# Optimization experiments

Measured on AMD Instinct MI355X. Metric: run time of the kernel, lower is better.

Reference implementation:

```python
import jax, jax.numpy as jnp
import numpy as np

E = 8        # num experts
K = 2        # top-k
H = 1024     # hidden size
F = 3584     # intermediate (ffn) size
B, S = 1, 2048


def setup_inputs() -> dict:
    key = jax.random.key(0)
    ks = jax.random.split(key, 5)
    scale_h = 1.0 / np.sqrt(H)
    scale_f = 1.0 / np.sqrt(F)
    return {
        "hidden_states": jax.random.normal(ks[0], (B, S, H), jnp.float32),
        "gate_w": jax.random.normal(ks[1], (E, H), jnp.float32) * scale_h,  # Linear [out,in]
        "w1": jax.random.normal(ks[2], (E, F, H), jnp.float32) * scale_h,
        "w3": jax.random.normal(ks[3], (E, F, H), jnp.float32) * scale_h,
        "w2": jax.random.normal(ks[4], (E, H, F), jnp.float32) * scale_f,
    }


def reference(hidden_states, gate_w, w1, w3, w2):
    b, s, h = hidden_states.shape
    x = hidden_states.reshape(-1, h)                       # [T,H]
    T = x.shape[0]
    # Router: softmax over experts, top-k, renormalize
    router_logits = x @ gate_w.T                           # [T,E]
    routing_weights = jax.nn.softmax(router_logits.astype(jnp.float32), axis=-1)
    topk_w, topk_idx = jax.lax.top_k(routing_weights, K)   # [T,K]
    topk_w = topk_w / jnp.sum(topk_w, axis=-1, keepdims=True)
    # Per-token, per-expert combine weight (0 for unselected experts) --
    # matches the original mask-and-sum over all experts.
    tok = jnp.arange(T)
    expert_weights = jnp.zeros((T, E), jnp.float32).at[tok[:, None], topk_idx].add(topk_w)  # [T,E]
    # Dense per-expert SiLU-gated MLP over all tokens (as the reference loop does),
    # vectorized across experts.
    g = jnp.einsum("th,efh->etf", x, w1)                   # [E,T,F]
    u = jnp.einsum("th,efh->etf", x, w3)                   # [E,T,F]
    act = jax.nn.silu(g) * u                               # [E,T,F]
    y = jnp.einsum("etf,ehf->eth", act, w2)                # [E,T,H]
    out = jnp.einsum("eth,te->th", y, expert_weights.astype(y.dtype))  # [T,H]
    return out.reshape(b, s, h)
```

## Files before the change

kernel.cpp:

```cpp
#include <hip/hip_runtime.h>
#include <hip/hip_bf16.h>

#define T_TOK 2048
#define HID   1024
#define FF    3584
#define NE    8
#define TOPK  2
#define GRIDY 24

typedef __bf16 bf16x8 __attribute__((ext_vector_type(8)));
typedef float  f32x4  __attribute__((ext_vector_type(4)));
typedef unsigned short u16x8 __attribute__((ext_vector_type(8)));

#define WS_COUNTS   0u
#define WS_OFFSETS  64u
#define WS_TILECNT  128u
#define WS_TLE      256u
#define WS_TLM      512u
#define WS_TOPKI    4096u
#define WS_TOPKW    20480u
#define WS_SLOTPOS  36864u
#define WS_SLOTROW  53248u
#define WS_ROUTETOK 69632u
#define WS_XG       131072u
#define WS_ACT      (WS_XG + 4096u*1024u*2u)
#define WS_Y        (WS_ACT + 4096u*3584u*2u)
#define Y_STRIDE    (4096u*1024u)

static __device__ __forceinline__ unsigned short f2bf(float f) {
    unsigned int u = __builtin_bit_cast(unsigned int, f);
    u += 0x7FFFu + ((u >> 16) & 1u);
    return (unsigned short)(u >> 16);
}
static __device__ __forceinline__ unsigned int cvtpk(float lo, float hi) {
    unsigned int r;
    asm("v_cvt_pk_bf16_f32 %0, %1, %2" : "=v"(r) : "v"(lo), "v"(hi));
    return r;
}

__global__ __launch_bounds__(256) void k_router(
    const float* __restrict__ x, const float* __restrict__ gw,
    int* __restrict__ counts, int* __restrict__ topki,
    float* __restrict__ topkw, int* __restrict__ slotpos)
{
    int t = blockIdx.x * 4 + (threadIdx.x >> 6);
    int l = threadIdx.x & 63;
    const float* xr = x + (size_t)t * HID;
    float acc[NE];
#pragma unroll
    for (int e = 0; e < NE; ++e) acc[e] = 0.f;
#pragma unroll
    for (int i = 0; i < 4; ++i) {
        int h = l * 4 + i * 256;
        float4 xv = *(const float4*)(xr + h);
#pragma unroll
        for (int e = 0; e < NE; ++e) {
            float4 g = *(const float4*)(gw + e * HID + h);
            acc[e] += xv.x * g.x + xv.y * g.y + xv.z * g.z + xv.w * g.w;
        }
    }
#pragma unroll
    for (int e = 0; e < NE; ++e) {
#pragma unroll
        for (int off = 32; off; off >>= 1) acc[e] += __shfl_xor(acc[e], off);
    }
    if (l == 0) {
        float best = -1e30f, second = -1e30f;
        int bi = 0, si = 0;
#pragma unroll
        for (int e = 0; e < NE; ++e) {
            float v = acc[e];
            if (v > best) { second = best; si = bi; best = v; bi = e; }
            else if (v > second) { second = v; si = e; }
        }
        float w0 = 1.f / (1.f + __expf(second - best));
        float w1 = 1.f - w0;
        topki[2 * t] = bi;  topki[2 * t + 1] = si;
        topkw[2 * t] = w0;  topkw[2 * t + 1] = w1;
        slotpos[2 * t]     = atomicAdd(&counts[bi], 1);
        slotpos[2 * t + 1] = atomicAdd(&counts[si], 1);
    }
}

__global__ void k_prefix(const int* __restrict__ counts, int* __restrict__ offsets,
                         int* __restrict__ tle, int* __restrict__ tlm,
                         int* __restrict__ tilecnt) {
    if (threadIdx.x == 0) {
        int o = 0;
#pragma unroll
        for (int e = 0; e < NE; ++e) { offsets[e] = o; o += counts[e]; }
        int n = 0;
        for (int e = 0; e < NE; ++e) {
            int t = (counts[e] + 255) >> 8;
            for (int i = 0; i < t; ++i) { tle[n] = e; tlm[n] = i; ++n; }
        }
        tilecnt[0] = n;
    }
}

__global__ void k_fill(const int* __restrict__ topki, const int* __restrict__ slotpos,
                       const int* __restrict__ offsets, int* __restrict__ routetok,
                       int* __restrict__ slotrow) {
    int j = blockIdx.x * blockDim.x + threadIdx.x;
    if (j >= T_TOK * TOPK) return;
    int e = topki[j];
    int row = offsets[e] + slotpos[j];
    routetok[row] = j >> 1;
    slotrow[j] = row;
}

__global__ void k_gather(const float* __restrict__ x, const int* __restrict__ routetok,
                         unsigned short* __restrict__ xg) {
    int j = blockIdx.x * blockDim.x + threadIdx.x;
    int r = j >> 8;
    int c = (j & 255) * 4;
    int tok = routetok[r];
    float4 v = *(const float4*)(x + (size_t)tok * HID + c);
    ushort4 o;
    o.x = f2bf(v.x); o.y = f2bf(v.y); o.z = f2bf(v.z); o.w = f2bf(v.w);
    int sc = c ^ ((r & 7) << 3);
    *(ushort4*)(xg + (size_t)r * HID + sc) = o;
}

__global__ __launch_bounds__(512, 4) void k_gemm1(
    const unsigned short* __restrict__ xg, const float* __restrict__ w1,
    const float* __restrict__ w3, const int* __restrict__ counts,
    const int* __restrict__ offsets, const int* __restrict__ tle,
    const int* __restrict__ tlm, const int* __restrict__ tilecnt,
    unsigned short* __restrict__ act)
{
    int by = blockIdx.y;
    if (by >= tilecnt[0]) return;
    int e = tle[by];
    int rbase = tlm[by] * 256;
    int cnt = counts[e], obase = offsets[e];
    int fbase = blockIdx.x * 64;

    __shared__ __align__(16) unsigned short lA[256 * 64];
    __shared__ __align__(16) unsigned short lB1[64 * 64];
    __shared__ __align__(16) unsigned short lB3[64 * 64];

    int tid = threadIdx.x;
    const int ra0 = tid >> 3, ca = (tid & 7) * 8;
    const int rb0 = tid >> 4, cb = (tid & 15) * 4;
    const unsigned short* pa[4];
#pragma unroll
    for (int i = 0; i < 4; ++i) {
        int r = obase + rbase + ra0 + 64 * i;
        if (r > 4095) r = 4095;
        pa[i] = xg + (size_t)r * HID + ca;
    }
    const float* w1e = w1 + ((size_t)e * FF + fbase) * HID;
    const float* w3e = w3 + ((size_t)e * FF + fbase) * HID;
    const float* pb1[2];
    const float* pb3[2];
    int wba[2];
#pragma unroll
    for (int i = 0; i < 2; ++i) {
        int row = rb0 + 32 * i;
        pb1[i] = w1e + (size_t)row * HID + cb;
        pb3[i] = w3e + (size_t)row * HID + cb;
        wba[i] = row * 64 + (cb ^ ((row & 7) << 3));
    }

    int lane = tid & 63, wv = tid >> 6, wr = wv >> 1, wc = wv & 1;
    int klane = (lane >> 4) * 8;
    int swzA = (((obase & 7) + (lane & 7)) & 7) << 3;
    int swzB = (lane & 7) << 3;
    f32x4 accg[4][2], accu[4][2];
#pragma unroll
    for (int m = 0; m < 4; ++m)
#pragma unroll
        for (int n = 0; n < 2; ++n) {
            accg[m][n] = (f32x4){0.f, 0.f, 0.f, 0.f};
            accu[m][n] = (f32x4){0.f, 0.f, 0.f, 0.f};
        }

    u16x8 ra[4]; float4 r1[2], r3[2];
#pragma unroll
    for (int i = 0; i < 4; ++i) ra[i] = *(const u16x8*)(pa[i]);
#pragma unroll
    for (int i = 0; i < 2; ++i) { r1[i] = *(const float4*)(pb1[i]); r3[i] = *(const float4*)(pb3[i]); }

    for (int kt = 0; kt < HID / 64; ++kt) {
#pragma unroll
        for (int i = 0; i < 4; ++i)
            *(u16x8*)(lA + (ra0 + 64 * i) * 64 + ca) = ra[i];
#pragma unroll
        for (int i = 0; i < 2; ++i) {
            uint2 p;
            p.x = cvtpk(r1[i].x, r1[i].y); p.y = cvtpk(r1[i].z, r1[i].w);
            *(uint2*)(lB1 + wba[i]) = p;
            p.x = cvtpk(r3[i].x, r3[i].y); p.y = cvtpk(r3[i].z, r3[i].w);
            *(uint2*)(lB3 + wba[i]) = p;
        }
        __syncthreads();
        if (kt < HID / 64 - 1) {
            int kof = (kt + 1) * 64;
#pragma unroll
            for (int i = 0; i < 4; ++i) ra[i] = *(const u16x8*)(pa[i] + kof);
#pragma unroll
            for (int i = 0; i < 2; ++i) {
                r1[i] = *(const float4*)(pb1[i] + kof);
                r3[i] = *(const float4*)(pb3[i] + kof);
            }
        }
#pragma unroll
        for (int kk = 0; kk < 64; kk += 32) {
            int kc = kk + klane;
            int kA = kc ^ swzA, kB = kc ^ swzB;
            bf16x8 a[4], b1[2], b3[2];
#pragma unroll
            for (int m = 0; m < 4; ++m)
                a[m] = *(const bf16x8*)(lA + (wr * 64 + m * 16 + (lane & 15)) * 64 + kA);
#pragma unroll
            for (int n = 0; n < 2; ++n) {
                b1[n] = *(const bf16x8*)(lB1 + (wc * 32 + n * 16 + (lane & 15)) * 64 + kB);
                b3[n] = *(const bf16x8*)(lB3 + (wc * 32 + n * 16 + (lane & 15)) * 64 + kB);
            }
#pragma unroll
            for (int m = 0; m < 4; ++m)
#pragma unroll
                for (int n = 0; n < 2; ++n) {
                    accg[m][n] = __builtin_amdgcn_mfma_f32_16x16x32_bf16(a[m], b1[n], accg[m][n], 0, 0, 0);
                    accu[m][n] = __builtin_amdgcn_mfma_f32_16x16x32_bf16(a[m], b3[n], accu[m][n], 0, 0, 0);
                }
        }
        __syncthreads();
    }

#pragma unroll
    for (int m = 0; m < 4; ++m)
#pragma unroll
        for (int n = 0; n < 2; ++n)
#pragma unroll
            for (int r = 0; r < 4; ++r) {
                int lr = wr * 64 + m * 16 + (lane >> 4) * 4 + r;
                if (rbase + lr < cnt) {
                    float g = accg[m][n][r], u = accu[m][n][r];
                    float s = g / (1.f + __expf(-g));
                    int row = obase + rbase + lr;
                    int col = fbase + wc * 32 + n * 16 + (lane & 15);
                    int scol = col ^ ((row & 7) << 3);
                    act[(size_t)row * FF + scol] = f2bf(s * u);
                }
            }
}

__global__ __launch_bounds__(512, 4) void k_gemm2(
    const unsigned short* __restrict__ act, const float* __restrict__ w2,
    const int* __restrict__ counts, const int* __restrict__ offsets,
    const int* __restrict__ tle, const int* __restrict__ tlm,
    const int* __restrict__ tilecnt, float* __restrict__ y)
{
    int by = blockIdx.y;
    if (by >= tilecnt[0]) return;
    int e = tle[by];
    int rbase = tlm[by] * 256;
    int cnt = counts[e], obase = offsets[e];
    int hbase = blockIdx.x * 64;
    int z = blockIdx.z;
    const int kb0 = z * (FF / 2);
    const int KS = FF / 2 / 64;

    __shared__ __align__(16) unsigned short lA[256 * 64];
    __shared__ __align__(16) unsigned short lB[64 * 64];

    int tid = threadIdx.x;
    const int ra0 = tid >> 3, ca = (tid & 7) * 8;
    const int rb0 = tid >> 4, cb = (tid & 15) * 4;
    const unsigned short* pa[4];
#pragma unroll
    for (int i = 0; i < 4; ++i) {
        int r = obase + rbase + ra0 + 64 * i;
        if (r > 4095) r = 4095;
        pa[i] = act + (size_t)r * FF + kb0 + ca;
    }
    const float* w2e = w2 + ((size_t)e * HID + hbase) * FF;
    const float* pb[2];
    int wba[2];
#pragma unroll
    for (int i = 0; i < 2; ++i) {
        int row = rb0 + 32 * i;
        pb[i] = w2e + (size_t)row * FF + kb0 + cb;
        wba[i] = row * 64 + (cb ^ ((row & 7) << 3));
    }

    int lane = tid & 63, wv = tid >> 6, wr = wv >> 1, wc = wv & 1;
    int klane = (lane >> 4) * 8;
    int swzA = (((obase & 7) + (lane & 7)) & 7) << 3;
    int swzB = (lane & 7) << 3;
    f32x4 acc[4][2];
#pragma unroll
    for (int m = 0; m < 4; ++m)
#pragma unroll
        for (int n = 0; n < 2; ++n) acc[m][n] = (f32x4){0.f, 0.f, 0.f, 0.f};

    u16x8 ra[4]; float4 rw[2];
#pragma unroll
    for (int i = 0; i < 4; ++i) ra[i] = *(const u16x8*)(pa[i]);
#pragma unroll
    for (int i = 0; i < 2; ++i) rw[i] = *(const float4*)(pb[i]);

    for (int kt = 0; kt < KS; ++kt) {
#pragma unroll
        for (int i = 0; i < 4; ++i)
            *(u16x8*)(lA + (ra0 + 64 * i) * 64 + ca) = ra[i];
#pragma unroll
        for (int i = 0; i < 2; ++i) {
            uint2 p;
            p.x = cvtpk(rw[i].x, rw[i].y); p.y = cvtpk(rw[i].z, rw[i].w);
            *(uint2*)(lB + wba[i]) = p;
        }
        __syncthreads();
        if (kt < KS - 1) {
            int kof = (kt + 1) * 64;
#pragma unroll
            for (int i = 0; i < 4; ++i) ra[i] = *(const u16x8*)(pa[i] + kof);
#pragma unroll
            for (int i = 0; i < 2; ++i) rw[i] = *(const float4*)(pb[i] + kof);
        }
#pragma unroll
        for (int kk = 0; kk < 64; kk += 32) {
            int kc = kk + klane;
            int kA = kc ^ swzA, kB = kc ^ swzB;
            bf16x8 a[4], b[2];
#pragma unroll
            for (int m = 0; m < 4; ++m)
                a[m] = *(const bf16x8*)(lA + (wr * 64 + m * 16 + (lane & 15)) * 64 + kA);
#pragma unroll
            for (int n = 0; n < 2; ++n)
                b[n] = *(const bf16x8*)(lB + (wc * 32 + n * 16 + (lane & 15)) * 64 + kB);
#pragma unroll
            for (int m = 0; m < 4; ++m)
#pragma unroll
                for (int n = 0; n < 2; ++n)
                    acc[m][n] = __builtin_amdgcn_mfma_f32_16x16x32_bf16(a[m], b[n], acc[m][n], 0, 0, 0);
        }
        __syncthreads();
    }

    float* yz = y + (size_t)z * Y_STRIDE;
#pragma unroll
    for (int m = 0; m < 4; ++m)
#pragma unroll
        for (int n = 0; n < 2; ++n)
#pragma unroll
            for (int r = 0; r < 4; ++r) {
                int lr = wr * 64 + m * 16 + (lane >> 4) * 4 + r;
                if (rbase + lr < cnt) {
                    int col = hbase + wc * 32 + n * 16 + (lane & 15);
                    yz[(size_t)(obase + rbase + lr) * HID + col] = acc[m][n][r];
                }
            }
}

__global__ void k_combine(const float* __restrict__ y, const int* __restrict__ slotrow,
                          const float* __restrict__ topkw, float* __restrict__ out) {
    int j = blockIdx.x * blockDim.x + threadIdx.x;
    int t = j >> 8, c = j & 255;
    int r0 = slotrow[2 * t], r1 = slotrow[2 * t + 1];
    float w0 = topkw[2 * t], w1 = topkw[2 * t + 1];
    const float4* y0 = (const float4*)y;
    const float4* y1 = (const float4*)(y + (size_t)Y_STRIDE);
    float4 a0 = y0[(size_t)r0 * 256 + c], a1 = y1[(size_t)r0 * 256 + c];
    float4 b0 = y0[(size_t)r1 * 256 + c], b1 = y1[(size_t)r1 * 256 + c];
    float4 o;
    o.x = w0 * (a0.x + a1.x) + w1 * (b0.x + b1.x);
    o.y = w0 * (a0.y + a1.y) + w1 * (b0.y + b1.y);
    o.z = w0 * (a0.z + a1.z) + w1 * (b0.z + b1.z);
    o.w = w0 * (a0.w + a1.w) + w1 * (b0.w + b1.w);
    ((float4*)out)[j] = o;
}

extern "C" void kernel_launch(void* const* d_in, const int* in_sizes, int n_in,
                              void* d_out, int out_size, void* d_ws, size_t ws_size,
                              hipStream_t stream) {
    const float* x  = (const float*)d_in[0];
    const float* gw = (const float*)d_in[1];
    const float* w1 = (const float*)d_in[2];
    const float* w3 = (const float*)d_in[3];
    const float* w2 = (const float*)d_in[4];
    float* out = (float*)d_out;

    char* ws = (char*)d_ws;
    int*   counts   = (int*)(ws + WS_COUNTS);
    int*   offsets  = (int*)(ws + WS_OFFSETS);
    int*   tilecnt  = (int*)(ws + WS_TILECNT);
    int*   tle      = (int*)(ws + WS_TLE);
    int*   tlm      = (int*)(ws + WS_TLM);
    int*   topki    = (int*)(ws + WS_TOPKI);
    float* topkw    = (float*)(ws + WS_TOPKW);
    int*   slotpos  = (int*)(ws + WS_SLOTPOS);
    int*   slotrow  = (int*)(ws + WS_SLOTROW);
    int*   routetok = (int*)(ws + WS_ROUTETOK);
    unsigned short* xg   = (unsigned short*)(ws + WS_XG);
    unsigned short* actb = (unsigned short*)(ws + WS_ACT);
    float* yb = (float*)(ws + WS_Y);

    hipMemsetAsync(counts, 0, 64, stream);
    k_router<<<T_TOK / 4, 256, 0, stream>>>(x, gw, counts, topki, topkw, slotpos);
    k_prefix<<<1, 64, 0, stream>>>(counts, offsets, tle, tlm, tilecnt);
    k_fill<<<16, 256, 0, stream>>>(topki, slotpos, offsets, routetok, slotrow);
    k_gather<<<4096, 256, 0, stream>>>(x, routetok, xg);
    k_gemm1<<<dim3(FF / 64, GRIDY, 1), 512, 0, stream>>>(xg, w1, w3, counts, offsets, tle, tlm, tilecnt, actb);
    k_gemm2<<<dim3(HID / 64, GRIDY, 2), 512, 0, stream>>>(actb, w2, counts, offsets, tle, tlm, tilecnt, yb);
    k_combine<<<2048, 256, 0, stream>>>(yb, slotrow, topkw, out);
}
```

Before: 279.0 us.

## Retile gemm2 to 128x128 tiles with configurable split-K

The down-projection kernel changes from 256x64 tiles with 512 threads to 128x128 tiles with 256 threads. It uses a separate 128-row tile list built in the prefix kernel and a split-K factor of 4 when the workspace is large enough. Each thread now loads 32 contiguous fp32 weights per k-step and writes them to LDS as packed 16-byte bf16 stores. The aim is to cut redundant w2 loads per output and add more blocks for occupancy. In exchange, the combine kernel must read and sum more partial y buffers.

```diff
diff --git a/kernel.cpp b/kernel.cpp
--- a/kernel.cpp
+++ b/kernel.cpp
@@ -6,7 +6,8 @@
 #define FF    3584
 #define NE    8
 #define TOPK  2
-#define GRIDY 24
+#define GRIDY1 24
+#define GRIDY2 40
 
 typedef __bf16 bf16x8 __attribute__((ext_vector_type(8)));
 typedef float  f32x4  __attribute__((ext_vector_type(4)));
@@ -15,8 +16,10 @@
 #define WS_COUNTS   0u
 #define WS_OFFSETS  64u
 #define WS_TILECNT  128u
-#define WS_TLE      256u
-#define WS_TLM      512u
+#define WS_TLE1     256u
+#define WS_TLM1     512u
+#define WS_TLE2     768u
+#define WS_TLM2     1024u
 #define WS_TOPKI    4096u
 #define WS_TOPKW    20480u
 #define WS_SLOTPOS  36864u
@@ -83,18 +86,21 @@
 }
 
 __global__ void k_prefix(const int* __restrict__ counts, int* __restrict__ offsets,
-                         int* __restrict__ tle, int* __restrict__ tlm,
+                         int* __restrict__ tl1e, int* __restrict__ tl1m,
+                         int* __restrict__ tl2e, int* __restrict__ tl2m,
                          int* __restrict__ tilecnt) {
     if (threadIdx.x == 0) {
         int o = 0;
 #pragma unroll
         for (int e = 0; e < NE; ++e) { offsets[e] = o; o += counts[e]; }
-        int n = 0;
+        int n1 = 0, n2 = 0;
         for (int e = 0; e < NE; ++e) {
-            int t = (counts[e] + 255) >> 8;
-            for (int i = 0; i < t; ++i) { tle[n] = e; tlm[n] = i; ++n; }
-        }
-        tilecnt[0] = n;
+            int t1 = (counts[e] + 255) >> 8;
+            for (int i = 0; i < t1; ++i) { tl1e[n1] = e; tl1m[n1] = i; ++n1; }
+            int t2 = (counts[e] + 127) >> 7;
+            for (int i = 0; i < t2; ++i) { tl2e[n2] = e; tl2m[n2] = i; ++n2; }
+        }
+        tilecnt[0] = n1; tilecnt[1] = n2;
     }
 }
 
@@ -247,94 +253,96 @@
             }
 }
 
-__global__ __launch_bounds__(512, 4) void k_gemm2(
+__global__ __launch_bounds__(256, 4) void k_gemm2(
     const unsigned short* __restrict__ act, const float* __restrict__ w2,
     const int* __restrict__ counts, const int* __restrict__ offsets,
     const int* __restrict__ tle, const int* __restrict__ tlm,
-    const int* __restrict__ tilecnt, float* __restrict__ y)
+    const int* __restrict__ tilecnt, float* __restrict__ y, int ks)
 {
     int by = blockIdx.y;
-    if (by >= tilecnt[0]) return;
+    if (by >= tilecnt[1]) return;
     int e = tle[by];
-    int rbase = tlm[by] * 256;
+    int rbase = tlm[by] * 128;
     int cnt = counts[e], obase = offsets[e];
-    int hbase = blockIdx.x * 64;
+    int hbase = blockIdx.x * 128;
     int z = blockIdx.z;
-    const int kb0 = z * (FF / 2);
-    const int KS = FF / 2 / 64;
-
-    __shared__ __align__(16) unsigned short lA[256 * 64];
-    __shared__ __align__(16) unsigned short lB[64 * 64];
+    const int KTOT = FF / 64;
+    int per = (KTOT + ks - 1) / ks;
+    int kt0 = z * per;
+    int ktn = (KTOT < kt0 + per ? KTOT : kt0 + per) - kt0;
+    int kb0 = kt0 * 64;
+
+    __shared__ __align__(16) unsigned short lA[128 * 64];
+    __shared__ __align__(16) unsigned short lB[128 * 64];
 
     int tid = threadIdx.x;
     const int ra0 = tid >> 3, ca = (tid & 7) * 8;
-    const int rb0 = tid >> 4, cb = (tid & 15) * 4;
     const unsigned short* pa[4];
 #pragma unroll
     for (int i = 0; i < 4; ++i) {
-        int r = obase + rbase + ra0 + 64 * i;
+        int r = obase + rbase + ra0 + 32 * i;
         if (r > 4095) r = 4095;
         pa[i] = act + (size_t)r * FF + kb0 + ca;
     }
-    const float* w2e = w2 + ((size_t)e * HID + hbase) * FF;
-    const float* pb[2];
-    int wba[2];
-#pragma unroll
-    for (int i = 0; i < 2; ++i) {
-        int row = rb0 + 32 * i;
-        pb[i] = w2e + (size_t)row * FF + kb0 + cb;
-        wba[i] = row * 64 + (cb ^ ((row & 7) << 3));
-    }
+    int hr = tid >> 1, kh = tid & 1;
+    const float* pb = w2 + ((size_t)e * HID + hbase + hr) * FF + kb0 + kh * 32;
+    int wba[4];
+#pragma unroll
+    for (int g = 0; g < 4; ++g)
+        wba[g] = hr * 64 + ((kh * 32 + g * 8) ^ ((hr & 7) << 3));
 
     int lane = tid & 63, wv = tid >> 6, wr = wv >> 1, wc = wv & 1;
     int klane = (lane >> 4) * 8;
     int swzA = (((obase & 7) + (lane & 7)) & 7) << 3;
     int swzB = (lane & 7) << 3;
-    f32x4 acc[4][2];
+    f32x4 acc[4][4];
 #pragma unroll
     for (int m = 0; m < 4; ++m)
 #pragma unroll
-        for (int n = 0; n < 2; ++n) acc[m][n] = (f32x4){0.f, 0.f, 0.f, 0.f};
-
-    u16x8 ra[4]; float4 rw[2];
+        for (int n = 0; n < 4; ++n) acc[m][n] = (f32x4){0.f, 0.f, 0.f, 0.f};
+
+    u16x8 ra[4]; float4 rw[8];
 #pragma unroll
     for (int i = 0; i < 4; ++i) ra[i] = *(const u16x8*)(pa[i]);
 #pragma unroll
-    for (int i = 0; i < 2; ++i) rw[i] = *(const float4*)(pb[i]);
-
-    for (int kt = 0; kt < KS; ++kt) {
+    for (int j = 0; j < 8; ++j) rw[j] = *(const float4*)(pb + 4 * j);
+
+    for (int kt = 0; kt < ktn; ++kt) {
 #pragma unroll
         for (int i = 0; i < 4; ++i)
-            *(u16x8*)(lA + (ra0 + 64 * i) * 64 + ca) = ra[i];
-#pragma unroll
-        for (int i = 0; i < 2; ++i) {
-            uint2 p;
-            p.x = cvtpk(rw[i].x, rw[i].y); p.y = cvtpk(rw[i].z, rw[i].w);
-            *(uint2*)(lB + wba[i]) = p;
+            *(u16x8*)(lA + (ra0 + 32 * i) * 64 + ca) = ra[i];
+#pragma unroll
+        for (int g = 0; g < 4; ++g) {
+            uint4 q;
+            q.x = cvtpk(rw[2 * g].x, rw[2 * g].y);
+            q.y = cvtpk(rw[2 * g].z, rw[2 * g].w);
+            q.z = cvtpk(rw[2 * g + 1].x, rw[2 * g + 1].y);
+            q.w = cvtpk(rw[2 * g + 1].z, rw[2 * g + 1].w);
+            *(uint4*)(lB + wba[g]) = q;
         }
         __syncthreads();
-        if (kt < KS - 1) {
+        if (kt < ktn - 1) {
             int kof = (kt + 1) * 64;
 #pragma unroll
             for (int i = 0; i < 4; ++i) ra[i] = *(const u16x8*)(pa[i] + kof);
 #pragma unroll
-            for (int i = 0; i < 2; ++i) rw[i] = *(const float4*)(pb[i] + kof);
+            for (int j = 0; j < 8; ++j) rw[j] = *(const float4*)(pb + kof + 4 * j);
         }
 #pragma unroll
         for (int kk = 0; kk < 64; kk += 32) {
             int kc = kk + klane;
             int kA = kc ^ swzA, kB = kc ^ swzB;
-            bf16x8 a[4], b[2];
+            bf16x8 a[4], b[4];
 #pragma unroll
             for (int m = 0; m < 4; ++m)
                 a[m] = *(const bf16x8*)(lA + (wr * 64 + m * 16 + (lane & 15)) * 64 + kA);
 #pragma unroll
-            for (int n = 0; n < 2; ++n)
-                b[n] = *(const bf16x8*)(lB + (wc * 32 + n * 16 + (lane & 15)) * 64 + kB);
+            for (int n = 0; n < 4; ++n)
+                b[n] = *(const bf16x8*)(lB + (wc * 64 + n * 16 + (lane & 15)) * 64 + kB);
 #pragma unroll
             for (int m = 0; m < 4; ++m)
 #pragma unroll
-                for (int n = 0; n < 2; ++n)
+                for (int n = 0; n < 4; ++n)
                     acc[m][n] = __builtin_amdgcn_mfma_f32_16x16x32_bf16(a[m], b[n], acc[m][n], 0, 0, 0);
         }
         __syncthreads();
@@ -344,32 +352,36 @@
 #pragma unroll
     for (int m = 0; m < 4; ++m)
 #pragma unroll
-        for (int n = 0; n < 2; ++n)
+        for (int n = 0; n < 4; ++n)
 #pragma unroll
             for (int r = 0; r < 4; ++r) {
                 int lr = wr * 64 + m * 16 + (lane >> 4) * 4 + r;
                 if (rbase + lr < cnt) {
-                    int col = hbase + wc * 32 + n * 16 + (lane & 15);
+                    int col = hbase + wc * 64 + n * 16 + (lane & 15);
                     yz[(size_t)(obase + rbase + lr) * HID + col] = acc[m][n][r];
                 }
             }
 }
 
 __global__ void k_combine(const float* __restrict__ y, const int* __restrict__ slotrow,
-                          const float* __restrict__ topkw, float* __restrict__ out) {
+                          const float* __restrict__ topkw, float* __restrict__ out, int ks) {
     int j = blockIdx.x * blockDim.x + threadIdx.x;
     int t = j >> 8, c = j & 255;
     int r0 = slotrow[2 * t], r1 = slotrow[2 * t + 1];
     float w0 = topkw[2 * t], w1 = topkw[2 * t + 1];
-    const float4* y0 = (const float4*)y;
-    const float4* y1 = (const float4*)(y + (size_t)Y_STRIDE);
-    float4 a0 = y0[(size_t)r0 * 256 + c], a1 = y1[(size_t)r0 * 256 + c];
-    float4 b0 = y0[(size_t)r1 * 256 + c], b1 = y1[(size_t)r1 * 256 + c];
+    float4 a = {0.f, 0.f, 0.f, 0.f}, b = {0.f, 0.f, 0.f, 0.f};
+    for (int z = 0; z < ks; ++z) {
+        const float4* yz = (const float4*)(y + (size_t)z * Y_STRIDE);
+        float4 av = yz[(size_t)r0 * 256 + c];
+        float4 bv = yz[(size_t)r1 * 256 + c];
+        a.x += av.x; a.y += av.y; a.z += av.z; a.w += av.w;
+        b.x += bv.x; b.y += bv.y; b.z += bv.z; b.w += bv.w;
+    }
     float4 o;
-    o.x = w0 * (a0.x + a1.x) + w1 * (b0.x + b1.x);
-    o.y = w0 * (a0.y + a1.y) + w1 * (b0.y + b1.y);
-    o.z = w0 * (a0.z + a1.z) + w1 * (b0.z + b1.z);
-    o.w = w0 * (a0.w + a1.w) + w1 * (b0.w + b1.w);
+    o.x = w0 * a.x + w1 * b.x;
+    o.y = w0 * a.y + w1 * b.y;
+    o.z = w0 * a.z + w1 * b.z;
+    o.w = w0 * a.w + w1 * b.w;
     ((float4*)out)[j] = o;
 }
 
@@ -387,8 +399,10 @@
     int*   counts   = (int*)(ws + WS_COUNTS);
     int*   offsets  = (int*)(ws + WS_OFFSETS);
     int*   tilecnt  = (int*)(ws + WS_TILECNT);
-    int*   tle      = (int*)(ws + WS_TLE);
-    int*   tlm      = (int*)(ws + WS_TLM);
+    int*   tl1e     = (int*)(ws + WS_TLE1);
+    int*   tl1m     = (int*)(ws + WS_TLM1);
+    int*   tl2e     = (int*)(ws + WS_TLE2);
+    int*   tl2m     = (int*)(ws + WS_TLM2);
     int*   topki    = (int*)(ws + WS_TOPKI);
     float* topkw    = (float*)(ws + WS_TOPKW);
     int*   slotpos  = (int*)(ws + WS_SLOTPOS);
@@ -398,12 +412,15 @@
     unsigned short* actb = (unsigned short*)(ws + WS_ACT);
     float* yb = (float*)(ws + WS_Y);
 
+    size_t ybytes = (size_t)Y_STRIDE * 4;
+    int ks = (ws_size >= (size_t)WS_Y + 4 * ybytes) ? 4 : 2;
+
     hipMemsetAsync(counts, 0, 64, stream);
     k_router<<<T_TOK / 4, 256, 0, stream>>>(x, gw, counts, topki, topkw, slotpos);
-    k_prefix<<<1, 64, 0, stream>>>(counts, offsets, tle, tlm, tilecnt);
+    k_prefix<<<1, 64, 0, stream>>>(counts, offsets, tl1e, tl1m, tl2e, tl2m, tilecnt);
     k_fill<<<16, 256, 0, stream>>>(topki, slotpos, offsets, routetok, slotrow);
     k_gather<<<4096, 256, 0, stream>>>(x, routetok, xg);
-    k_gemm1<<<dim3(FF / 64, GRIDY, 1), 512, 0, stream>>>(xg, w1, w3, counts, offsets, tle, tlm, tilecnt, actb);
-    k_gemm2<<<dim3(HID / 64, GRIDY, 2), 512, 0, stream>>>(actb, w2, counts, offsets, tle, tlm, tilecnt, yb);
-    k_combine<<<2048, 256, 0, stream>>>(yb, slotrow, topkw, out);
-}
+    k_gemm1<<<dim3(FF / 64, GRIDY1, 1), 512, 0, stream>>>(xg, w1, w3, counts, offsets, tl1e, tl1m, tilecnt, actb);
+    k_gemm2<<<dim3(HID / 128, GRIDY2, ks), 256, 0, stream>>>(actb, w2, counts, offsets, tl2e, tl2m, tilecnt, yb, ks);
+    k_combine<<<2048, 256, 0, stream>>>(yb, slotrow, topkw, out, ks);
+}
```

New measurement: 391.1 us. 1.4x slower.
